# Kernel optimization log

Measured on AMD Instinct MI355X. Metric: run time of the kernel, lower is better.

The kernel has to match this reference:

```python
import jax, jax.numpy as jnp
import numpy as np

DN = ('NCHW', 'OIHW', 'NCHW')

def conv3x3(x, w, b):
    y = jax.lax.conv_general_dilated(x, w, window_strides=(1, 1), padding='SAME', dimension_numbers=DN)
    return y + b[None, :, None, None]

def setup_inputs() -> dict:
    key = jax.random.key(0)
    ks = jax.random.split(key, 12)
    B, C, H, W, r = 4, 64, 128, 128, 2
    ic = C * r * r  # 256
    s = 0.02
    inp = {
        'x': jax.random.normal(ks[0], (B, C, H, W), jnp.float32),
        'g_w': jax.random.normal(ks[1], (ic, ic), jnp.float32) * s,
        'g_b': jnp.zeros((ic,), jnp.float32),
        'theta_w': jax.random.normal(ks[2], (ic, ic), jnp.float32) * s,
        'theta_b': jnp.zeros((ic,), jnp.float32),
        'phi_w': jax.random.normal(ks[3], (ic, ic), jnp.float32) * s,
        'phi_b': jnp.zeros((ic,), jnp.float32),
        'Ws_w': jax.random.normal(ks[4], (C, C), jnp.float32) * s,
        'Ws_b': jnp.zeros((C,), jnp.float32),
        'Wc_w': jax.random.normal(ks[5], (C, C), jnp.float32) * s,
        'Wc_b': jnp.zeros((C,), jnp.float32),
        'gamma_s': jnp.ones((1,), jnp.float32),
        'gamma_c': jnp.ones((1,), jnp.float32),
        'm1_w': jax.random.normal(ks[6], (16, C, 3, 3), jnp.float32) * s,
        'm1_b': jnp.zeros((16,), jnp.float32),
        'm2_w': jax.random.normal(ks[7], (1, 16, 3, 3), jnp.float32) * s,
        'm2_b': jnp.zeros((1,), jnp.float32),
    }
    return inp

def reference(x, g_w, g_b, theta_w, theta_b, phi_w, phi_b, Ws_w, Ws_b, Wc_w, Wc_b, gamma_s, gamma_c, m1_w, m1_b, m2_w, m2_b):
    b, c, h, w = x.shape
    ic = g_w.shape[0]
    r = int(round((ic // c) ** 0.5))
    hr, wr = h // r, w // r
    n = hr * wr  # spatial positions after channel-folding
    # x1: [b, ic, n] (row-major reshape, same as torch .reshape)
    x1 = x.reshape(b, ic, n)
    # 1x1 convs == channel matmuls
    g_x = jnp.einsum('oi,bin->bno', g_w, x1) + g_b          # [b, n, ic]
    th = jnp.einsum('oi,bin->bon', theta_w, x1) + theta_b[:, None]  # [b, ic, n]
    ph = jnp.einsum('oi,bin->bon', phi_w, x1) + phi_b[:, None]      # [b, ic, n]
    # spatial attention: [b, n, n]
    f_s = jnp.einsum('bcn,bcm->bnm', th, ph)
    f_s = jax.nn.softmax(f_s, axis=-1)
    y_s = jnp.einsum('bnm,bmo->bno', f_s, g_x)              # [b, n, ic]
    y_s = jnp.transpose(y_s, (0, 2, 1)).reshape(b, c, h, w)
    # channel attention: [b, ic, ic]
    f_c = jnp.einsum('bcn,bdn->bcd', th, ph)
    f_c = jax.nn.softmax(f_c, axis=-1)
    y_c = jnp.einsum('bno,bod->bnd', g_x, f_c).reshape(b, c, h, w)
    ws = jnp.einsum('oi,bihw->bohw', Ws_w, y_s) + Ws_b[None, :, None, None]
    wc = jnp.einsum('oi,bihw->bohw', Wc_w, y_c) + Wc_b[None, :, None, None]
    z = x + gamma_s[0] * ws + gamma_c[0] * wc
    hmid = jax.nn.relu(conv3x3(z, m1_w, m1_b))
    logit = conv3x3(hmid, m2_w, m2_b)
    return (logit, z)
```

## Files before the change

### kernel.cpp

```cpp
#include <hip/hip_runtime.h>
#include <stdint.h>

typedef unsigned short u16;
typedef unsigned int   u32;

typedef __attribute__((ext_vector_type(8)))  short bf16x8;
typedef __attribute__((ext_vector_type(4)))  float f32x4;
typedef __attribute__((ext_vector_type(4)))  unsigned int u32x4;

__device__ __forceinline__ float b2f(u16 u) { return __uint_as_float(((u32)u) << 16); }
__device__ __forceinline__ float blo(u32 u) { return __uint_as_float(u << 16); }
__device__ __forceinline__ float bhi(u32 u) { return __uint_as_float(u & 0xffff0000u); }
__device__ __forceinline__ u16 f2b(float f) {
    u32 x = __float_as_uint(f);
    u32 r = (x + 0x7fffu + ((x >> 16) & 1u)) >> 16;
    return (u16)r;
}

#define NB   4
#define IC   256
#define NPOS 4096
#define CH   64
#define HW   16384

__global__ __launch_bounds__(256) void prep_kernel(
    const float* __restrict__ wsw, const float* __restrict__ wcw,
    const float* __restrict__ m1w,
    const float* __restrict__ thw, const float* __restrict__ phw, const float* __restrict__ gw,
    float* __restrict__ wswT, float* __restrict__ wcwT, float* __restrict__ m1wT,
    u16* __restrict__ wbf)
{
    int idx = blockIdx.x * 256 + threadIdx.x;
    if (idx < 65536) {
        wbf[idx]          = f2b(thw[idx]);
        wbf[idx + 65536]  = f2b(phw[idx]);
        wbf[idx + 131072] = f2b(gw[idx]);
    }
    if (idx < 4096) {
        int i = idx >> 6, c = idx & 63;
        wswT[i*64 + c] = wsw[c*64 + i];
        wcwT[i*64 + c] = wcw[c*64 + i];
    }
    if (idx < 9216) {
        int o = idx & 15, ct = idx >> 4;
        int t = ct % 9, c = ct / 9;
        m1wT[idx] = m1w[(o*64 + c)*9 + t];
    }
}

__global__ __launch_bounds__(256) void qkv_mfma_kernel(
    const float* __restrict__ x, const u16* __restrict__ wbf,
    const float* __restrict__ thb, const float* __restrict__ phb, const float* __restrict__ gb,
    u16* __restrict__ Q, u16* __restrict__ K, u16* __restrict__ VT)
{
    __shared__ __align__(16) u32 xT[64*132];
    __shared__ __align__(16) float bias_l[256];
    const int tid  = threadIdx.x;
    const int w    = tid >> 6;
    const int lane = tid & 63;
    const int q4   = lane >> 4;
    const int l    = lane & 15;
    const int n0   = blockIdx.x * 64;
    const int b    = blockIdx.y;
    const int mat  = blockIdx.z;
    const u16* wmat = wbf + mat * 65536;
    const float* bias = (mat == 0) ? thb : (mat == 1) ? phb : gb;

    bias_l[tid] = bias[tid];

    {
        const float* xb = x + ((size_t)b*IC)*NPOS + n0;
        int n   = tid & 63;
        int ip0 = tid >> 6;
        #pragma unroll 4
        for (int p=0; p<32; p++){
            int ip = ip0 + p*4;
            float v0 = xb[(size_t)(2*ip  )*NPOS + n];
            float v1 = xb[(size_t)(2*ip+1)*NPOS + n];
            xT[n*132 + ip] = (u32)f2b(v0) | ((u32)f2b(v1) << 16);
        }
    }
    __syncthreads();

    f32x4 acc[4][4];
    #pragma unroll
    for (int ot=0; ot<4; ot++)
        #pragma unroll
        for (int nt=0; nt<4; nt++) acc[ot][nt] = (f32x4){0.f,0.f,0.f,0.f};

    #pragma unroll
    for (int f=0; f<8; f++){
        bf16x8 bfrag[4];
        #pragma unroll
        for (int nt=0; nt<4; nt++)
            bfrag[nt] = *(const bf16x8*)&xT[(nt*16 + l)*132 + f*16 + q4*4];
        #pragma unroll
        for (int ot=0; ot<4; ot++){
            bf16x8 afrag = *(const bf16x8*)(wmat + (size_t)(w*64 + ot*16 + l)*256 + f*32 + q4*8);
            #pragma unroll
            for (int nt=0; nt<4; nt++)
                acc[ot][nt] = __builtin_amdgcn_mfma_f32_16x16x32_bf16(afrag, bfrag[nt], acc[ot][nt], 0, 0, 0);
        }
    }
    __syncthreads();

    if (mat < 2){
        u16* zbuf = (u16*)xT;
        #pragma unroll
        for (int nt=0; nt<4; nt++)
            #pragma unroll
            for (int ot=0; ot<4; ot++){
                int o = w*64 + ot*16 + q4*4;
                float4 bv = *(const float4*)&bias_l[o];
                uint2 pk;
                pk.x = (u32)f2b(acc[ot][nt][0]+bv.x) | ((u32)f2b(acc[ot][nt][1]+bv.y) << 16);
                pk.y = (u32)f2b(acc[ot][nt][2]+bv.z) | ((u32)f2b(acc[ot][nt][3]+bv.w) << 16);
                *(uint2*)&zbuf[(nt*16 + l)*264 + o] = pk;
            }
        __syncthreads();
        u16* dst = ((mat == 0) ? Q : K) + ((size_t)(b*NPOS + n0))*IC;
        int n = tid >> 2, o0 = (tid & 3)*64;
        const u32* src = &xT[n*132 + (tid & 3)*32];
        #pragma unroll
        for (int m=0; m<8; m++)
            *(uint4*)(dst + (size_t)n*IC + o0 + m*8) = ((const uint4*)src)[m];
    } else {
        u16* zbuf = (u16*)xT;
        #pragma unroll
        for (int nt=0; nt<4; nt++)
            #pragma unroll
            for (int ot=0; ot<4; ot++){
                int o = w*64 + ot*16 + q4*4;
                int n = nt*16 + l;
                #pragma unroll
                for (int reg=0; reg<4; reg++)
                    zbuf[(o+reg)*66 + n] = f2b(acc[ot][nt][reg] + bias_l[o+reg]);
            }
        __syncthreads();
        const u32* src = &xT[tid*33];
        u32 tmp[32];
        #pragma unroll
        for (int m=0; m<32; m++) tmp[m] = src[m];
        u16* dst = VT + ((size_t)(b*IC + tid))*NPOS + n0;
        #pragma unroll
        for (int m=0; m<8; m++){
            uint4 v; v.x = tmp[m*4]; v.y = tmp[m*4+1]; v.z = tmp[m*4+2]; v.w = tmp[m*4+3];
            *(uint4*)(dst + m*8) = v;
        }
    }
}

__global__ __launch_bounds__(256) void fc_mfma_kernel(
    const u16* __restrict__ Q, const u16* __restrict__ K, float* __restrict__ fcp)
{
    __shared__ __align__(16) u16 QT[64*72];
    __shared__ __align__(16) u16 KT[64*72];
    const int tid = threadIdx.x;
    const int w   = tid >> 6;
    const int lane = tid & 63;
    const int q4  = lane >> 4;
    const int l   = lane & 15;
    const int c0  = blockIdx.x * 64;
    const int d0  = blockIdx.y * 64;
    const int b   = blockIdx.z >> 2;
    const int nseg= blockIdx.z & 3;

    f32x4 acc[4];
    #pragma unroll
    for (int dt=0; dt<4; dt++) acc[dt] = (f32x4){0.f,0.f,0.f,0.f};

    for (int chunk=0; chunk<16; chunk++){
        const int n0 = nseg*1024 + chunk*64;
        __syncthreads();
        {
            int r  = tid >> 2;
            int cq = (tid & 3) * 16;
            const u16* qs = Q + ((size_t)(b*NPOS + n0 + r))*IC + c0 + cq;
            const u16* ks = K + ((size_t)(b*NPOS + n0 + r))*IC + d0 + cq;
            u16 qv[16], kv[16];
            *(uint4*)&qv[0] = *(const uint4*)qs;
            *(uint4*)&qv[8] = *(const uint4*)(qs + 8);
            *(uint4*)&kv[0] = *(const uint4*)ks;
            *(uint4*)&kv[8] = *(const uint4*)(ks + 8);
            #pragma unroll
            for (int j=0;j<16;j++){
                QT[(cq+j)*72 + r] = qv[j];
                KT[(cq+j)*72 + r] = kv[j];
            }
        }
        __syncthreads();
        #pragma unroll
        for (int f=0; f<2; f++){
            bf16x8 af = *(const bf16x8*)&QT[(w*16 + l)*72 + f*32 + q4*8];
            #pragma unroll
            for (int dt=0; dt<4; dt++){
                bf16x8 bf2 = *(const bf16x8*)&KT[(dt*16 + l)*72 + f*32 + q4*8];
                acc[dt] = __builtin_amdgcn_mfma_f32_16x16x32_bf16(af, bf2, acc[dt], 0, 0, 0);
            }
        }
    }

    #pragma unroll
    for (int dt=0; dt<4; dt++)
        #pragma unroll
        for (int reg=0; reg<4; reg++)
            fcp[((size_t)((nseg*NB + b)*256 + c0 + w*16 + q4*4 + reg))*256 + d0 + dt*16 + l] = acc[dt][reg];
}

__global__ __launch_bounds__(256) void softmax_fc_kernel(
    const float* __restrict__ fcp, u16* __restrict__ pcb)
{
    __shared__ float red[8];
    const int tid = threadIdx.x;
    const int b = blockIdx.x >> 8, c = blockIdx.x & 255;
    float v = 0.f;
    #pragma unroll
    for (int s=0; s<4; s++)
        v += fcp[((size_t)((s*NB + b)*256 + c))*256 + tid];
    float m = v;
    #pragma unroll
    for (int d=32; d>=1; d>>=1) m = fmaxf(m, __shfl_xor(m, d));
    if ((tid & 63) == 0) red[tid>>6] = m;
    __syncthreads();
    m = fmaxf(fmaxf(red[0],red[1]), fmaxf(red[2],red[3]));
    float e = __expf(v - m);
    float s = e;
    #pragma unroll
    for (int d=32; d>=1; d>>=1) s += __shfl_xor(s, d);
    if ((tid & 63) == 0) red[4 + (tid>>6)] = s;
    __syncthreads();
    s = red[4]+red[5]+red[6]+red[7];
    pcb[(size_t)b*65536 + (size_t)c*256 + tid] = f2b(e / s);
}

__global__ __launch_bounds__(256) void yc_mfma_kernel(
    const u16* __restrict__ VT, const u16* __restrict__ pcb, u16* __restrict__ ycb)
{
    __shared__ __align__(16) u16 Vl[64*32];
    __shared__ __align__(16) u16 Pcl[64*32];
    const int tid = threadIdx.x;
    const int w = tid >> 6, lane = tid & 63;
    const int q4 = lane >> 4, l = lane & 15;
    const int n0 = blockIdx.x * 64, d0 = blockIdx.y * 64, b = blockIdx.z;

    f32x4 acc[4];
    #pragma unroll
    for (int dt=0; dt<4; dt++) acc[dt] = (f32x4){0.f,0.f,0.f,0.f};

    const int so = tid >> 3;
    const int sj = tid & 7;

    for (int oc=0; oc<8; oc++){
        const int o0 = oc*32;
        __syncthreads();
        {
            uint4 v = *(const uint4*)(VT + ((size_t)(b*IC + o0 + so))*NPOS + n0 + sj*8);
            u16 tv[8]; *(uint4*)tv = v;
            #pragma unroll
            for (int m=0;m<8;m++){
                int n = sj*8 + m;
                Vl[n*32 + ((((so>>3) ^ (n&3)))<<3) + (so&7)] = tv[m];
            }
            uint4 pv = *(const uint4*)(pcb + (size_t)b*65536 + (size_t)(o0 + so)*256 + d0 + sj*8);
            u16 tp[8]; *(uint4*)tp = pv;
            #pragma unroll
            for (int m=0;m<8;m++){
                int d = sj*8 + m;
                Pcl[d*32 + ((((so>>3) ^ (d&3)))<<3) + (so&7)] = tp[m];
            }
        }
        __syncthreads();
        bf16x8 af = *(const bf16x8*)&Vl[(w*16 + l)*32 + ((q4 ^ (l&3))<<3)];
        #pragma unroll
        for (int dt=0; dt<4; dt++){
            bf16x8 bfr = *(const bf16x8*)&Pcl[(dt*16 + l)*32 + ((q4 ^ (l&3))<<3)];
            acc[dt] = __builtin_amdgcn_mfma_f32_16x16x32_bf16(af, bfr, acc[dt], 0, 0, 0);
        }
    }

    #pragma unroll
    for (int dt=0; dt<4; dt++)
        #pragma unroll
        for (int reg=0; reg<4; reg++)
            ycb[((size_t)(b*NPOS + n0 + w*16 + q4*4 + reg))*IC + d0 + dt*16 + l] = f2b(acc[dt][reg]);
}

__global__ __launch_bounds__(256) void flash_mfma_kernel(
    const u16* __restrict__ Q, const u16* __restrict__ K, const u16* __restrict__ VT,
    u16* __restrict__ opart0, u16* __restrict__ opartx, float* __restrict__ lpart,
    int sshift)
{
    __shared__ __align__(16) u32 Kt[8192];
    __shared__ __align__(16) u32 Vt[8192];
    __shared__ __align__(16) u16 Pl[4608];
    const int tid  = threadIdx.x;
    const int w    = tid >> 6;
    const int lane = tid & 63;
    const int q4   = lane >> 4;
    const int l    = lane & 15;
    const int S    = 1 << sshift;

    const int id   = blockIdx.x;
    const int xcd  = id & 7;
    const int b    = xcd >> 1;
    const int h    = xcd & 1;
    const int r    = id >> 3;
    const int n0   = ((r & 31) | (h << 5)) * 64;
    const int seg  = r >> 5;
    const int tiles = 64 >> sshift;
    const int kt0   = seg * tiles;

    bf16x8 qf[8];
    {
        const u16* qrow = Q + ((size_t)(b*NPOS + n0 + w*16 + l))*IC;
        #pragma unroll
        for (int f=0; f<8; f++){
            u32x4 qv = __builtin_nontemporal_load((const u32x4*)(qrow + f*32 + q4*8));
            qf[f] = *(bf16x8*)&qv;
        }
    }

    f32x4 oacc[16];
    #pragma unroll
    for (int t=0;t<16;t++) oacc[t] = (f32x4){0.f,0.f,0.f,0.f};
    float lrow[4] = {0.f, 0.f, 0.f, 0.f};

    u16* Pz = Pl + w*1152;

    auto stage_k = [&](int m0s){
        #pragma unroll
        for (int j=0;j<8;j++){
            int call = w*8 + j;
            int rr = call*2 + (lane>>5);
            int c = (lane & 31) ^ (rr & 7);
            const u16* g = K + ((size_t)(b*NPOS + m0s + rr))*IC + c*8;
            __builtin_amdgcn_global_load_lds(
                (const __attribute__((address_space(1))) u32*)(const void*)g,
                (__attribute__((address_space(3))) u32*)(void*)&Kt[call*256], 16, 0, 0);
        }
    };
    auto stage_v = [&](int m0s){
        #pragma unroll
        for (int j=0;j<8;j++){
            int call = w*8 + j;
            int d = call*8 + (lane>>3);
            int c = (lane & 7) ^ (d & 7);
            const u16* g = VT + ((size_t)(b*IC + d))*NPOS + m0s + c*8;
            __builtin_amdgcn_global_load_lds(
                (const __attribute__((address_space(1))) u32*)(const void*)g,
                (__attribute__((address_space(3))) u32*)(void*)&Vt[call*256], 16, 0, 0);
        }
    };

    stage_k(kt0*64);
    stage_v(kt0*64);
    asm volatile("s_waitcnt vmcnt(0)" ::: "memory");
    __builtin_amdgcn_sched_barrier(0);
    __builtin_amdgcn_s_barrier();
    __builtin_amdgcn_sched_barrier(0);

    for (int kti=0; kti<tiles; kti++){
        const bool more = (kti + 1 < tiles);
        const int mn = (kt0 + kti + 1)*64;

        f32x4 sac[4];
        #pragma unroll
        for (int t=0;t<4;t++) sac[t] = (f32x4){0.f,0.f,0.f,0.f};
        __builtin_amdgcn_s_setprio(1);
        #pragma unroll
        for (int f=0; f<8; f++){
            #pragma unroll
            for (int t=0;t<4;t++){
                int rr = t*16 + l;
                int c = (f*4 + q4) ^ (rr & 7);
                bf16x8 kf = *(const bf16x8*)((const u16*)Kt + rr*256 + c*8);
                sac[t] = __builtin_amdgcn_mfma_f32_16x16x32_bf16(qf[f], kf, sac[t], 0, 0, 0);
            }
        }
        __builtin_amdgcn_s_setprio(0);

        __builtin_amdgcn_sched_barrier(0);
        __builtin_amdgcn_s_barrier();
        __builtin_amdgcn_sched_barrier(0);

        if (more) stage_k(mn);

        #pragma unroll
        for (int reg=0; reg<4; reg++){
            float p0 = __expf(sac[0][reg]), p1 = __expf(sac[1][reg]);
            float p2 = __expf(sac[2][reg]), p3 = __expf(sac[3][reg]);
            lrow[reg] += (p0+p1) + (p2+p3);
            int m = q4*4 + reg;
            Pz[m*72 + l]      = f2b(p0);
            Pz[m*72 + 16 + l] = f2b(p1);
            Pz[m*72 + 32 + l] = f2b(p2);
            Pz[m*72 + 48 + l] = f2b(p3);
        }

        if (more) { asm volatile("s_waitcnt vmcnt(8)" ::: "memory"); }
        else      { asm volatile("s_waitcnt vmcnt(0)" ::: "memory"); }
        __builtin_amdgcn_sched_barrier(0);
        __builtin_amdgcn_s_barrier();
        __builtin_amdgcn_sched_barrier(0);

        __builtin_amdgcn_s_setprio(1);
        #pragma unroll
        for (int s2=0; s2<2; s2++){
            bf16x8 pa = *(const bf16x8*)(Pz + l*72 + s2*32 + q4*8);
            #pragma unroll
            for (int t=0;t<16;t++){
                int d = t*16 + l;
                int c = (s2*4 + q4) ^ (d & 7);
                bf16x8 vb = *(const bf16x8*)((const u16*)Vt + d*64 + c*8);
                oacc[t] = __builtin_amdgcn_mfma_f32_16x16x32_bf16(pa, vb, oacc[t], 0, 0, 0);
            }
        }
        __builtin_amdgcn_s_setprio(0);

        __builtin_amdgcn_sched_barrier(0);
        __builtin_amdgcn_s_barrier();
        __builtin_amdgcn_sched_barrier(0);

        if (more) {
            stage_v(mn);
            asm volatile("s_waitcnt vmcnt(8)" ::: "memory");
        } else {
            asm volatile("s_waitcnt vmcnt(0)" ::: "memory");
        }
        __builtin_amdgcn_sched_barrier(0);
        __builtin_amdgcn_s_barrier();
        __builtin_amdgcn_sched_barrier(0);
    }

    #pragma unroll
    for (int reg=0; reg<4; reg++){
        float v = lrow[reg];
        v += __shfl_xor(v, 1); v += __shfl_xor(v, 2);
        v += __shfl_xor(v, 4); v += __shfl_xor(v, 8);
        if (l == 0)
            lpart[((size_t)(seg*NB + b))*NPOS + n0 + w*16 + q4*4 + reg] = v;
    }

    __syncthreads();
    u16* Ez = (u16*)Kt + w*4096;
    #pragma unroll
    for (int t=0;t<16;t++)
        #pragma unroll
        for (int reg=0;reg<4;reg++)
            Ez[(t*16 + l)*16 + q4*4 + reg] = f2b(oacc[t][reg]);
    u16* base = (seg == 0) ? opart0 : (opartx + (size_t)(seg-1)*((size_t)NB*IC*NPOS));
    u16* dst = base + (size_t)b*(IC*NPOS) + n0 + w*16;
    for (int p=0; p<32; p++){
        int d = p*8 + (lane>>3);
        u32 val = *(const u32*)(Ez + d*16 + (lane&7)*2);
        __builtin_nontemporal_store(val, (u32*)(dst + (size_t)d*NPOS + (lane&7)*2));
    }
}

__global__ __launch_bounds__(256) void z_kernel(
    const float* __restrict__ x,
    const u16* __restrict__ opart0, const u16* __restrict__ opartx,
    const float* __restrict__ lpart, int S,
    const u16* __restrict__ ycb,
    const float* __restrict__ wswT, const float* __restrict__ wcwT,
    const float* __restrict__ wsb, const float* __restrict__ wcb,
    const float* __restrict__ gs, const float* __restrict__ gc,
    float* __restrict__ zout)
{
    __shared__ __align__(16) float Wsl[64*32];
    __shared__ __align__(16) float Wcl[64*32];
    __shared__ __align__(16) float rlL[256];
    __shared__ __align__(16) u16 ysl[32*264];
    __shared__ __align__(16) u16 ycl[32*264];
    const int tid = threadIdx.x;
    const int p = blockIdx.x * 256 + tid;
    const int cbase = blockIdx.y * 32;
    const int b = blockIdx.z;
    {
        int i = tid >> 2, c8 = (tid & 3) * 8;
        const float* s1 = wswT + i*64 + cbase + c8;
        const float* s2 = wcwT + i*64 + cbase + c8;
        *(float4*)&Wsl[i*32 + c8]     = *(const float4*)s1;
        *(float4*)&Wsl[i*32 + c8 + 4] = *(const float4*)(s1+4);
        *(float4*)&Wcl[i*32 + c8]     = *(const float4*)s2;
        *(float4*)&Wcl[i*32 + c8 + 4] = *(const float4*)(s2+4);
    }
    {
        float Ls = 0.f;
        for (int s=0; s<S; s++)
            Ls += lpart[((size_t)(s*NB + b))*NPOS + (p & 4095)];
        rlL[tid] = 1.f / Ls;
    }

    float as[32], ac[32];
    #pragma unroll
    for (int c=0;c<32;c++){ as[c]=0.f; ac[c]=0.f; }

    const size_t CHUNK = (size_t)NB*IC*NPOS;
    const size_t bbase = (size_t)b*(IC*NPOS) + (size_t)blockIdx.x*256;

    for (int half=0; half<2; half++){
        __syncthreads();
        #pragma unroll
        for (int k=0;k<4;k++){
            int ci  = tid + k*256;
            int il  = ci >> 5;
            int i   = half*32 + il;
            int oct = ci & 31;
            size_t gidx = bbase + (size_t)i*HW + oct*8;
            float y8[8] = {0,0,0,0,0,0,0,0};
            for (int s=0;s<S;s++){
                const u16* psrc = (s==0) ? opart0 : (opartx + (size_t)(s-1)*CHUNK);
                uint4 v = *(const uint4*)(psrc + gidx);
                y8[0]+=blo(v.x); y8[1]+=bhi(v.x); y8[2]+=blo(v.y); y8[3]+=bhi(v.y);
                y8[4]+=blo(v.z); y8[5]+=bhi(v.z); y8[6]+=blo(v.w); y8[7]+=bhi(v.w);
            }
            u32 pk[4];
            #pragma unroll
            for (int j=0;j<4;j++){
                float a0 = y8[2*j]   * rlL[oct*8 + 2*j];
                float a1 = y8[2*j+1] * rlL[oct*8 + 2*j+1];
                pk[j] = (u32)f2b(a0) | ((u32)f2b(a1) << 16);
            }
            *(uint4*)&ysl[il*264 + oct*8] = *(uint4*)pk;
            uint4 vc = *(const uint4*)(ycb + gidx);
            *(uint4*)&ycl[il*264 + oct*8] = vc;
        }
        __syncthreads();
        for (int il=0; il<32; il++){
            int i = half*32 + il;
            float ysv = b2f(ysl[il*264 + tid]);
            float ycv = b2f(ycl[il*264 + tid]);
            #pragma unroll
            for (int c=0;c<32;c++){
                as[c] = fmaf(Wsl[i*32+c], ysv, as[c]);
                ac[c] = fmaf(Wcl[i*32+c], ycv, ac[c]);
            }
        }
    }

    float gsv = gs[0], gcv = gc[0];
    #pragma unroll
    for (int c=0;c<32;c++){
        int cg = cbase + c;
        float xv = x[((size_t)b*CH + cg)*HW + p];
        float zv = fmaf(gsv, as[c] + wsb[cg], xv);
        zv = fmaf(gcv, ac[c] + wcb[cg], zv);
        zout[((size_t)b*CH + cg)*HW + p] = zv;
    }
}

__global__ __launch_bounds__(256) void conv1_kernel(
    const float* __restrict__ z, const float* __restrict__ m1wT, const float* __restrict__ m1b,
    float* __restrict__ hmid)
{
    const int tid = threadIdx.x;
    const int p = blockIdx.x * 128 + (tid & 127);
    const int oh = (tid >> 7) * 8;
    const int b = blockIdx.y;
    const int y = p >> 7, xx = p & 127;
    float acc[8];
    #pragma unroll
    for (int o=0;o<8;o++) acc[o]=0.f;
    for (int c=0;c<64;c++){
        const float* zp = z + ((size_t)b*CH + c)*HW;
        #pragma unroll
        for (int t=0;t<9;t++){
            int dy = t/3 - 1, dx = t%3 - 1;
            int yy = y + dy, xv = xx + dx;
            float zv = 0.f;
            if (yy >= 0 && yy < 128 && xv >= 0 && xv < 128) zv = zp[yy*128 + xv];
            const float* w = m1wT + (c*9 + t)*16 + oh;
            #pragma unroll
            for (int o=0;o<8;o++) acc[o] = fmaf(w[o], zv, acc[o]);
        }
    }
    #pragma unroll
    for (int o=0;o<8;o++)
        hmid[((size_t)b*16 + oh + o)*HW + p] = fmaxf(acc[o] + m1b[oh + o], 0.f);
}

__global__ __launch_bounds__(256) void conv2_kernel(
    const float* __restrict__ hmid, const float* __restrict__ m2w, const float* __restrict__ m2b,
    float* __restrict__ logit)
{
    const int idx = blockIdx.x * 256 + threadIdx.x;
    const int b = idx >> 14, p = idx & 16383;
    const int y = p >> 7, xx = p & 127;
    float acc = 0.f;
    for (int c=0;c<16;c++){
        const float* hp = hmid + ((size_t)b*16 + c)*HW;
        #pragma unroll
        for (int t=0;t<9;t++){
            int dy = t/3 - 1, dx = t%3 - 1;
            int yy = y + dy, xv = xx + dx;
            if (yy >= 0 && yy < 128 && xv >= 0 && xv < 128)
                acc = fmaf(m2w[c*9+t], hp[yy*128 + xv], acc);
        }
    }
    logit[idx] = acc + m2b[0];
}

extern "C" void kernel_launch(void* const* d_in, const int* in_sizes, int n_in,
                              void* d_out, int out_size, void* d_ws, size_t ws_size,
                              hipStream_t stream)
{
    const float* x    = (const float*)d_in[0];
    const float* g_w  = (const float*)d_in[1];
    const float* g_b  = (const float*)d_in[2];
    const float* th_w = (const float*)d_in[3];
    const float* th_b = (const float*)d_in[4];
    const float* ph_w = (const float*)d_in[5];
    const float* ph_b = (const float*)d_in[6];
    const float* ws_w = (const float*)d_in[7];
    const float* ws_b = (const float*)d_in[8];
    const float* wc_w = (const float*)d_in[9];
    const float* wc_b = (const float*)d_in[10];
    const float* gs   = (const float*)d_in[11];
    const float* gc   = (const float*)d_in[12];
    const float* m1w  = (const float*)d_in[13];
    const float* m1b  = (const float*)d_in[14];
    const float* m2w  = (const float*)d_in[15];
    const float* m2b  = (const float*)d_in[16];

    char* ws = (char*)d_ws;
    u16*   Qb   = (u16*)  (ws + 0);
    u16*   Kb   = (u16*)  (ws + 8388608);
    u16*   VTb  = (u16*)  (ws + 16777216);
    u16*   ysT  = (u16*)  (ws + 25165824);
    u16*   ycb  = (u16*)  (ws + 33554432);
    u16*   wbf  = (u16*)  (ws + 41943040);
    u16*   pcb  = (u16*)  (ws + 42991616);
    float* fcp  = (float*)(ws + 44040192);
    float* hmid = (float*)(ws + 44040192);
    float* lpart= (float*)(ws + 44040192);
    float* wswT = (float*)(ws + 48234496);
    float* wcwT = (float*)(ws + 48250880);
    float* m1wT = (float*)(ws + 48267264);
    u16*   opartx = (u16*)(ws + 48304128);

    float* logit = (float*)d_out;
    float* zout  = (float*)d_out + 65536;

    int sshift = 0;
    if (ws_size >= 48304128ULL + 3ULL*8388608ULL)      sshift = 2;
    else if (ws_size >= 48304128ULL + 1ULL*8388608ULL) sshift = 1;

    prep_kernel<<<256, 256, 0, stream>>>(ws_w, wc_w, m1w, th_w, ph_w, g_w,
                                         wswT, wcwT, m1wT, wbf);
    qkv_mfma_kernel<<<dim3(64,4,3), 256, 0, stream>>>(x, wbf, th_b, ph_b, g_b, Qb, Kb, VTb);
    fc_mfma_kernel<<<dim3(4,4,16), 256, 0, stream>>>(Qb, Kb, fcp);
    softmax_fc_kernel<<<1024, 256, 0, stream>>>(fcp, pcb);
    yc_mfma_kernel<<<dim3(64,4,4), 256, 0, stream>>>(VTb, pcb, ycb);
    flash_mfma_kernel<<<dim3(NB * 64 * (1 << sshift)), 256, 0, stream>>>(Qb, Kb, VTb, ysT, opartx, lpart, sshift);
    z_kernel<<<dim3(64,2,4), 256, 0, stream>>>(x, ysT, opartx, lpart, 1 << sshift, ycb,
                                               wswT, wcwT, ws_b, wc_b, gs, gc, zout);
    conv1_kernel<<<dim3(128,4), 256, 0, stream>>>(zout, m1wT, m1b, hmid);
    conv2_kernel<<<256, 256, 0, stream>>>(hmid, m2w, m2b, logit);
}
```

Before: 407.8 us.

## Halve flash key tile to 32, split fc over more segments, vectorize x load

```diff
diff --git a/kernel.cpp b/kernel.cpp
--- a/kernel.cpp
+++ b/kernel.cpp
@@ -69,15 +69,18 @@
     bias_l[tid] = bias[tid];
 
     {
-        const float* xb = x + ((size_t)b*IC)*NPOS + n0;
-        int n   = tid & 63;
-        int ip0 = tid >> 6;
+        u16* xT16 = (u16*)xT;
+        const int rq = tid >> 4;
+        const int nq = tid & 15;
+        const float* xb = x + ((size_t)b*IC)*NPOS + n0 + nq*4;
         #pragma unroll 4
-        for (int p=0; p<32; p++){
-            int ip = ip0 + p*4;
-            float v0 = xb[(size_t)(2*ip  )*NPOS + n];
-            float v1 = xb[(size_t)(2*ip+1)*NPOS + n];
-            xT[n*132 + ip] = (u32)f2b(v0) | ((u32)f2b(v1) << 16);
+        for (int p2=0; p2<16; p2++){
+            int i = p2*16 + rq;
+            float4 v = *(const float4*)(xb + (size_t)i*NPOS);
+            xT16[(nq*4+0)*264 + i] = f2b(v.x);
+            xT16[(nq*4+1)*264 + i] = f2b(v.y);
+            xT16[(nq*4+2)*264 + i] = f2b(v.z);
+            xT16[(nq*4+3)*264 + i] = f2b(v.w);
         }
     }
     __syncthreads();
@@ -151,7 +154,8 @@
 }
 
 __global__ __launch_bounds__(256) void fc_mfma_kernel(
-    const u16* __restrict__ Q, const u16* __restrict__ K, float* __restrict__ fcp)
+    const u16* __restrict__ Q, const u16* __restrict__ K, float* __restrict__ fcp,
+    int nslg)
 {
     __shared__ __align__(16) u16 QT[64*72];
     __shared__ __align__(16) u16 KT[64*72];
@@ -162,15 +166,16 @@
     const int l   = lane & 15;
     const int c0  = blockIdx.x * 64;
     const int d0  = blockIdx.y * 64;
-    const int b   = blockIdx.z >> 2;
-    const int nseg= blockIdx.z & 3;
+    const int b   = blockIdx.z >> nslg;
+    const int ns  = blockIdx.z & ((1 << nslg) - 1);
+    const int chunks = 64 >> nslg;
 
     f32x4 acc[4];
     #pragma unroll
     for (int dt=0; dt<4; dt++) acc[dt] = (f32x4){0.f,0.f,0.f,0.f};
 
-    for (int chunk=0; chunk<16; chunk++){
-        const int n0 = nseg*1024 + chunk*64;
+    for (int chunk=0; chunk<chunks; chunk++){
+        const int n0 = (ns*chunks + chunk)*64;
         __syncthreads();
         {
             int r  = tid >> 2;
@@ -204,18 +209,17 @@
     for (int dt=0; dt<4; dt++)
         #pragma unroll
         for (int reg=0; reg<4; reg++)
-            fcp[((size_t)((nseg*NB + b)*256 + c0 + w*16 + q4*4 + reg))*256 + d0 + dt*16 + l] = acc[dt][reg];
+            fcp[((size_t)((ns*NB + b)*256 + c0 + w*16 + q4*4 + reg))*256 + d0 + dt*16 + l] = acc[dt][reg];
 }
 
 __global__ __launch_bounds__(256) void softmax_fc_kernel(
-    const float* __restrict__ fcp, u16* __restrict__ pcb)
+    const float* __restrict__ fcp, u16* __restrict__ pcb, int nsegs)
 {
     __shared__ float red[8];
     const int tid = threadIdx.x;
     const int b = blockIdx.x >> 8, c = blockIdx.x & 255;
     float v = 0.f;
-    #pragma unroll
-    for (int s=0; s<4; s++)
+    for (int s=0; s<nsegs; s++)
         v += fcp[((size_t)((s*NB + b)*256 + c))*256 + tid];
     float m = v;
     #pragma unroll
@@ -290,9 +294,10 @@
     u16* __restrict__ opart0, u16* __restrict__ opartx, float* __restrict__ lpart,
     int sshift)
 {
-    __shared__ __align__(16) u32 Kt[8192];
-    __shared__ __align__(16) u32 Vt[8192];
-    __shared__ __align__(16) u16 Pl[4608];
+    __shared__ __align__(16) u32 lds[9472];
+    u32* Kt = lds;
+    u32* Vt = lds + 4096;
+    u16* Pl = (u16*)(lds + 8192);
     const int tid  = threadIdx.x;
     const int w    = tid >> 6;
     const int lane = tid & 63;
@@ -307,7 +312,7 @@
     const int r    = id >> 3;
     const int n0   = ((r & 31) | (h << 5)) * 64;
     const int seg  = r >> 5;
-    const int tiles = 64 >> sshift;
+    const int tiles = 128 >> sshift;
     const int kt0   = seg * tiles;
 
     bf16x8 qf[8];
@@ -325,12 +330,12 @@
     for (int t=0;t<16;t++) oacc[t] = (f32x4){0.f,0.f,0.f,0.f};
     float lrow[4] = {0.f, 0.f, 0.f, 0.f};
 
-    u16* Pz = Pl + w*1152;
+    u16* Pz = Pl + w*640;
 
     auto stage_k = [&](int m0s){
         #pragma unroll
-        for (int j=0;j<8;j++){
-            int call = w*8 + j;
+        for (int j=0;j<4;j++){
+            int call = w*4 + j;
             int rr = call*2 + (lane>>5);
             int c = (lane & 31) ^ (rr & 7);
             const u16* g = K + ((size_t)(b*NPOS + m0s + rr))*IC + c*8;
@@ -341,10 +346,10 @@
     };
     auto stage_v = [&](int m0s){
         #pragma unroll
-        for (int j=0;j<8;j++){
-            int call = w*8 + j;
-            int d = call*8 + (lane>>3);
-            int c = (lane & 7) ^ (d & 7);
+        for (int j=0;j<4;j++){
+            int call = w*4 + j;
+            int d = call*16 + (lane>>2);
+            int c = (lane & 3) ^ (d & 3);
             const u16* g = VT + ((size_t)(b*IC + d))*NPOS + m0s + c*8;
             __builtin_amdgcn_global_load_lds(
                 (const __attribute__((address_space(1))) u32*)(const void*)g,
@@ -352,8 +357,8 @@
         }
     };
 
-    stage_k(kt0*64);
-    stage_v(kt0*64);
+    stage_k(kt0*32);
+    stage_v(kt0*32);
     asm volatile("s_waitcnt vmcnt(0)" ::: "memory");
     __builtin_amdgcn_sched_barrier(0);
     __builtin_amdgcn_s_barrier();
@@ -361,16 +366,16 @@
 
     for (int kti=0; kti<tiles; kti++){
         const bool more = (kti + 1 < tiles);
-        const int mn = (kt0 + kti + 1)*64;
-
-        f32x4 sac[4];
-        #pragma unroll
-        for (int t=0;t<4;t++) sac[t] = (f32x4){0.f,0.f,0.f,0.f};
+        const int mn = (kt0 + kti + 1)*32;
+
+        f32x4 sac[2];
+        sac[0] = (f32x4){0.f,0.f,0.f,0.f};
+        sac[1] = (f32x4){0.f,0.f,0.f,0.f};
         __builtin_amdgcn_s_setprio(1);
         #pragma unroll
         for (int f=0; f<8; f++){
             #pragma unroll
-            for (int t=0;t<4;t++){
+            for (int t=0;t<2;t++){
                 int rr = t*16 + l;
                 int c = (f*4 + q4) ^ (rr & 7);
                 bf16x8 kf = *(const bf16x8*)((const u16*)Kt + rr*256 + c*8);
@@ -388,30 +393,26 @@
         #pragma unroll
         for (int reg=0; reg<4; reg++){
             float p0 = __expf(sac[0][reg]), p1 = __expf(sac[1][reg]);
-            float p2 = __expf(sac[2][reg]), p3 = __expf(sac[3][reg]);
-            lrow[reg] += (p0+p1) + (p2+p3);
+            lrow[reg] += p0 + p1;
             int m = q4*4 + reg;
-            Pz[m*72 + l]      = f2b(p0);
-            Pz[m*72 + 16 + l] = f2b(p1);
-            Pz[m*72 + 32 + l] = f2b(p2);
-            Pz[m*72 + 48 + l] = f2b(p3);
-        }
-
-        if (more) { asm volatile("s_waitcnt vmcnt(8)" ::: "memory"); }
+            Pz[m*40 + l]      = f2b(p0);
+            Pz[m*40 + 16 + l] = f2b(p1);
+        }
+
+        if (more) { asm volatile("s_waitcnt vmcnt(4)" ::: "memory"); }
         else      { asm volatile("s_waitcnt vmcnt(0)" ::: "memory"); }
         __builtin_amdgcn_sched_barrier(0);
         __builtin_amdgcn_s_barrier();
         __builtin_amdgcn_sched_barrier(0);
 
         __builtin_amdgcn_s_setprio(1);
-        #pragma unroll
-        for (int s2=0; s2<2; s2++){
-            bf16x8 pa = *(const bf16x8*)(Pz + l*72 + s2*32 + q4*8);
+        {
+            bf16x8 pa = *(const bf16x8*)(Pz + l*40 + q4*8);
             #pragma unroll
             for (int t=0;t<16;t++){
                 int d = t*16 + l;
-                int c = (s2*4 + q4) ^ (d & 7);
-                bf16x8 vb = *(const bf16x8*)((const u16*)Vt + d*64 + c*8);
+                int cc = q4 ^ (d & 3);
+                bf16x8 vb = *(const bf16x8*)((const u16*)Vt + d*32 + cc*8);
                 oacc[t] = __builtin_amdgcn_mfma_f32_16x16x32_bf16(pa, vb, oacc[t], 0, 0, 0);
             }
         }
@@ -423,7 +424,7 @@
 
         if (more) {
             stage_v(mn);
-            asm volatile("s_waitcnt vmcnt(8)" ::: "memory");
+            asm volatile("s_waitcnt vmcnt(4)" ::: "memory");
         } else {
             asm volatile("s_waitcnt vmcnt(0)" ::: "memory");
         }
@@ -442,7 +443,7 @@
     }
 
     __syncthreads();
-    u16* Ez = (u16*)Kt + w*4096;
+    u16* Ez = (u16*)lds + w*4096;
     #pragma unroll
     for (int t=0;t<16;t++)
         #pragma unroll
@@ -631,7 +632,7 @@
     u16*   ycb  = (u16*)  (ws + 33554432);
     u16*   wbf  = (u16*)  (ws + 41943040);
     u16*   pcb  = (u16*)  (ws + 42991616);
-    float* fcp  = (float*)(ws + 44040192);
+    float* fcp4 = (float*)(ws + 44040192);
     float* hmid = (float*)(ws + 44040192);
     float* lpart= (float*)(ws + 44040192);
     float* wswT = (float*)(ws + 48234496);
@@ -646,11 +647,14 @@
     if (ws_size >= 48304128ULL + 3ULL*8388608ULL)      sshift = 2;
     else if (ws_size >= 48304128ULL + 1ULL*8388608ULL) sshift = 1;
 
+    int nslg = (sshift >= 1) ? 3 : 2;
+    float* fcp = (sshift >= 1) ? (float*)(ws + 48304128) : fcp4;
+
     prep_kernel<<<256, 256, 0, stream>>>(ws_w, wc_w, m1w, th_w, ph_w, g_w,
                                          wswT, wcwT, m1wT, wbf);
     qkv_mfma_kernel<<<dim3(64,4,3), 256, 0, stream>>>(x, wbf, th_b, ph_b, g_b, Qb, Kb, VTb);
-    fc_mfma_kernel<<<dim3(4,4,16), 256, 0, stream>>>(Qb, Kb, fcp);
-    softmax_fc_kernel<<<1024, 256, 0, stream>>>(fcp, pcb);
+    fc_mfma_kernel<<<dim3(4,4,NB << nslg), 256, 0, stream>>>(Qb, Kb, fcp, nslg);
+    softmax_fc_kernel<<<1024, 256, 0, stream>>>(fcp, pcb, 1 << nslg);
     yc_mfma_kernel<<<dim3(64,4,4), 256, 0, stream>>>(VTb, pcb, ycb);
     flash_mfma_kernel<<<dim3(NB * 64 * (1 << sshift)), 256, 0, stream>>>(Qb, Kb, VTb, ysT, opartx, lpart, sshift);
     z_kernel<<<dim3(64,2,4), 256, 0, stream>>>(x, ysT, opartx, lpart, 1 << sshift, ycb,
```

Measured after the change: 427.4 us. 1.05x slower.
